# Optimization experiments

Hardware: AMD Instinct MI355X
Metric: run time of the kernel (lower is better)

## Reference

```python
import jax, jax.numpy as jnp
import numpy as np

EPS = 1e-6

def _rms(x, w):
    # RMSNorm over last dim with learned scale w
    var = jnp.mean(x * x, axis=-1, keepdims=True)
    return x * jax.lax.rsqrt(var + EPS) * w

def _split_heads(x, h):
    b, l, hd = x.shape
    return x.reshape(b, l, h, hd // h).transpose(0, 2, 1, 3)  # b h l d

def setup_inputs() -> dict:
    key = jax.random.key(0)
    ks = jax.random.split(key, 12)
    D = 2048          # hidden_size == ip_hidden_states_dim
    H = 16            # n_heads
    Dh = 128          # head_dim
    T = 1280          # timesteps_emb_dim
    B, L, Lip = 2, 2048, 512
    s = 0.02
    return {
        "ip_hidden_states": jax.random.normal(ks[0], (B, Lip, D), jnp.float32),
        "img_query": jax.random.normal(ks[1], (B, L, D), jnp.float32),
        "img_key": jax.random.normal(ks[2], (B, L, D), jnp.float32),
        "img_value": jax.random.normal(ks[3], (B, L, D), jnp.float32),
        "t_emb": jax.random.normal(ks[4], (B, T), jnp.float32),
        "W_ada": jax.random.normal(ks[5], (2 * D, T), jnp.float32) * s,
        "b_ada": jax.random.normal(ks[6], (2 * D,), jnp.float32) * s,
        "W_k_ip": jax.random.normal(ks[7], (D, D), jnp.float32) * s,
        "W_v_ip": jax.random.normal(ks[8], (D, D), jnp.float32) * s,
        "w_q": jnp.ones((Dh,), jnp.float32),
        "w_k": jnp.ones((Dh,), jnp.float32),
        "w_ipk": jnp.ones((Dh,), jnp.float32),
        "n_heads": H,
    }

def reference(ip_hidden_states, img_query, img_key, img_value, t_emb,
              W_ada, b_ada, W_k_ip, W_v_ip, w_q, w_k, w_ipk, n_heads):
    D = img_query.shape[-1]
    # AdaLayerNorm (mode='normal'): silu -> linear -> shift/scale, LN(no affine)
    emb = jax.nn.silu(t_emb) @ W_ada.T + b_ada          # [B, 2D]
    shift, scale = emb[:, :D], emb[:, D:]
    x = ip_hidden_states
    mu = jnp.mean(x, axis=-1, keepdims=True)
    var = jnp.mean((x - mu) ** 2, axis=-1, keepdims=True)
    xn = (x - mu) * jax.lax.rsqrt(var + 1e-6)
    ip_n = xn * (1.0 + scale[:, None, :]) + shift[:, None, :]
    # K/V projections for IP tokens
    ip_key = ip_n @ W_k_ip.T
    ip_value = ip_n @ W_v_ip.T
    # split heads
    q = _split_heads(img_query, n_heads)   # b h L d
    k = _split_heads(img_key, n_heads)
    v = _split_heads(img_value, n_heads)
    kip = _split_heads(ip_key, n_heads)    # b h Lip d
    vip = _split_heads(ip_value, n_heads)
    # RMSNorms
    q = _rms(q, w_q)
    k = _rms(k, w_k)
    kip = _rms(kip, w_ipk)
    # concat image + IP along sequence
    kcat = jnp.concatenate([k, kip], axis=2)
    vcat = jnp.concatenate([v, vip], axis=2)
    # SDPA
    d = q.shape[-1]
    scores = jnp.einsum('bhld,bhmd->bhlm', q, kcat) / jnp.sqrt(jnp.asarray(d, q.dtype))
    attn = jax.nn.softmax(scores, axis=-1)
    out = jnp.einsum('bhlm,bhmd->bhld', attn, vcat)
    b, h, l, dh = out.shape
    return out.transpose(0, 2, 1, 3).reshape(b, l, h * dh)
```

## Files before the change

kernel.cpp:

```cpp
#include <hip/hip_runtime.h>
#include <hip/hip_bf16.h>

typedef __attribute__((ext_vector_type(8))) __bf16 bf16x8;
typedef __attribute__((ext_vector_type(2))) __bf16 bf16x2;
typedef __attribute__((ext_vector_type(4))) float floatx4;
typedef __attribute__((ext_vector_type(2))) unsigned int uint2v;

#define DEV static __device__ __forceinline__

typedef __attribute__((address_space(1))) const unsigned int gu32;
typedef __attribute__((address_space(3))) unsigned int lu32;

DEV void dma16(const void* g, void* l) {
  __builtin_amdgcn_global_load_lds((gu32*)g, (lu32*)l, 16, 0, 0);
}

DEV unsigned short f2bf(float f) {
  unsigned int u = __float_as_uint(f);
  u += 0x7fffu + ((u >> 16) & 1u);
  return (unsigned short)(u >> 16);
}

DEV unsigned int pk_bf16(float a, float b) {
#if __has_builtin(__builtin_amdgcn_cvt_pk_bf16_f32)
  bf16x2 r = __builtin_amdgcn_cvt_pk_bf16_f32(a, b);
  union { bf16x2 v; unsigned int u; } c; c.v = r;
  return c.u;
#else
  return (unsigned int)f2bf(a) | ((unsigned int)f2bf(b) << 16);
#endif
}

DEV float wred_sum(float v) {
#pragma unroll
  for (int o = 32; o > 0; o >>= 1) v += __shfl_xor(v, o, 64);
  return v;
}

DEV floatx4 mfma32(bf16x8 a, bf16x8 b, floatx4 c) {
  return __builtin_amdgcn_mfma_f32_16x16x32_bf16(a, b, c, 0, 0, 0);
}

#if __has_builtin(__builtin_amdgcn_permlane32_swap) && __has_builtin(__builtin_amdgcn_permlane16_swap)
#define HAS_PLSWAP 1
DEV void p32sw(unsigned int& a, unsigned int& b) {
  uint2v r = __builtin_amdgcn_permlane32_swap(a, b, false, false);
  a = r[0]; b = r[1];
}
DEV void p16sw(unsigned int& a, unsigned int& b) {
  uint2v r = __builtin_amdgcn_permlane16_swap(a, b, false, false);
  a = r[0]; b = r[1];
}
#endif

__global__ void ada_kernel(const float* __restrict__ t_emb, const float* __restrict__ W_ada,
                           const float* __restrict__ b_ada, float* __restrict__ emb) {
  int w = threadIdx.x >> 6, lane = threadIdx.x & 63;
  int gid = blockIdx.x * 4 + w;
  int b = gid >> 12, n = gid & 4095;
  const float* te = t_emb + (size_t)b * 1280;
  const float* wr = W_ada + (size_t)n * 1280;
  float acc = 0.f;
#pragma unroll
  for (int i = 0; i < 20; ++i) {
    int t = lane + i * 64;
    float x = te[t];
    float s = x / (1.f + __expf(-x));
    acc += s * wr[t];
  }
  acc = wred_sum(acc);
  if (lane == 0) emb[gid] = acc + b_ada[n];
}

__global__ void ln_mod_kernel(const float* __restrict__ ip, const float* __restrict__ emb,
                              unsigned short* __restrict__ ipn) {
  int row = blockIdx.x;
  int b = row >> 9;
  const float* x = ip + (size_t)row * 2048;
  float xv[8];
  float s1 = 0.f, s2 = 0.f;
#pragma unroll
  for (int i = 0; i < 8; ++i) {
    float v = x[threadIdx.x + i * 256];
    xv[i] = v; s1 += v; s2 += v * v;
  }
  s1 = wred_sum(s1); s2 = wred_sum(s2);
  __shared__ float r1[4], r2[4];
  int w = threadIdx.x >> 6, lane = threadIdx.x & 63;
  if (lane == 0) { r1[w] = s1; r2[w] = s2; }
  __syncthreads();
  s1 = r1[0] + r1[1] + r1[2] + r1[3];
  s2 = r2[0] + r2[1] + r2[2] + r2[3];
  float mu = s1 * (1.f / 2048.f);
  float var = s2 * (1.f / 2048.f) - mu * mu;
  float rs = rsqrtf(var + 1e-6f);
  const float* sh = emb + (size_t)b * 4096;
  unsigned short* y = ipn + (size_t)row * 2048;
#pragma unroll
  for (int i = 0; i < 8; ++i) {
    int d = threadIdx.x + i * 256;
    float v = (xv[i] - mu) * rs;
    v = v * (1.f + sh[2048 + d]) + sh[d];
    y[d] = f2bf(v);
  }
}

struct us4 { unsigned short a, b, c, d; };
__global__ void cvtw_kernel(const float* __restrict__ wk, const float* __restrict__ wv,
                            unsigned short* __restrict__ wk16, unsigned short* __restrict__ wv16) {
  size_t i = ((size_t)blockIdx.x * 256 + threadIdx.x) * 4;
  float4 a = *(const float4*)(wk + i);
  float4 b = *(const float4*)(wv + i);
  us4 oa = { f2bf(a.x), f2bf(a.y), f2bf(a.z), f2bf(a.w) };
  us4 ob = { f2bf(b.x), f2bf(b.y), f2bf(b.z), f2bf(b.w) };
  *(us4*)(wk16 + i) = oa;
  *(us4*)(wv16 + i) = ob;
}

__global__ __launch_bounds__(256) void proj_gemm(const unsigned short* __restrict__ A,
    const unsigned short* __restrict__ Wk, const unsigned short* __restrict__ Wv,
    float* __restrict__ Ck, float* __restrict__ Cv) {
  const unsigned short* Bm = blockIdx.z ? Wv : Wk;
  float* C = blockIdx.z ? Cv : Ck;
  int n0 = blockIdx.x * 64, m0 = blockIdx.y * 128;
  __shared__ __align__(16) unsigned short As[128 * 72];
  __shared__ __align__(16) unsigned short Bs[64 * 72];
  int tid = threadIdx.x, w = tid >> 6, lane = tid & 63, quad = lane >> 4, l16 = lane & 15;
  floatx4 acc[2][4];
#pragma unroll
  for (int i = 0; i < 2; ++i)
#pragma unroll
    for (int j = 0; j < 4; ++j) { floatx4 z = {0.f, 0.f, 0.f, 0.f}; acc[i][j] = z; }
  for (int kk = 0; kk < 2048; kk += 64) {
#pragma unroll
    for (int it = 0; it < 4; ++it) {
      int idx = tid + it * 256;
      int row = idx >> 3, chk = idx & 7;
      *(uint4*)&As[row * 72 + chk * 8] = *(const uint4*)&A[(size_t)(m0 + row) * 2048 + kk + chk * 8];
    }
#pragma unroll
    for (int it = 0; it < 2; ++it) {
      int idx = tid + it * 256;
      int row = idx >> 3, chk = idx & 7;
      *(uint4*)&Bs[row * 72 + chk * 8] = *(const uint4*)&Bm[(size_t)(n0 + row) * 2048 + kk + chk * 8];
    }
    __syncthreads();
#pragma unroll
    for (int c = 0; c < 2; ++c) {
      bf16x8 a0 = *(const bf16x8*)&As[(w * 32 + l16) * 72 + quad * 8 + c * 32];
      bf16x8 a1 = *(const bf16x8*)&As[(w * 32 + 16 + l16) * 72 + quad * 8 + c * 32];
#pragma unroll
      for (int nt = 0; nt < 4; ++nt) {
        bf16x8 bb = *(const bf16x8*)&Bs[(nt * 16 + l16) * 72 + quad * 8 + c * 32];
        acc[0][nt] = mfma32(a0, bb, acc[0][nt]);
        acc[1][nt] = mfma32(a1, bb, acc[1][nt]);
      }
    }
    __syncthreads();
  }
#pragma unroll
  for (int rt = 0; rt < 2; ++rt)
#pragma unroll
    for (int nt = 0; nt < 4; ++nt)
#pragma unroll
      for (int r = 0; r < 4; ++r)
        C[(size_t)(m0 + w * 32 + rt * 16 + quad * 4 + r) * 2048 + n0 + nt * 16 + l16] = acc[rt][nt][r];
}

__global__ __launch_bounds__(256) void kv_build(const float* __restrict__ img_key, const float* __restrict__ img_value,
                         const float* __restrict__ ipk, const float* __restrict__ ipv,
                         const float* __restrict__ w_k, const float* __restrict__ w_ipk,
                         unsigned short* __restrict__ Kc, unsigned short* __restrict__ VtT) {
  int bh = blockIdx.x;
  int mt = blockIdx.y;
  int b = bh >> 4, hh = bh & 15;
  int m0 = mt * 64;
  __shared__ __align__(16) unsigned short Vs[64 * 132];
  int tid = threadIdx.x;
  int mrow = tid >> 2, dq = tid & 3;
  int m = m0 + mrow;
  size_t base;
  const float* wsrc;
  const float *ksrc, *vsrc;
  if (m < 2048) {
    base = (size_t)(b * 2048 + m) * 2048 + hh * 128;
    ksrc = img_key + base; vsrc = img_value + base; wsrc = w_k;
  } else {
    base = (size_t)(b * 512 + (m - 2048)) * 2048 + hh * 128;
    ksrc = ipk + base; vsrc = ipv + base; wsrc = w_ipk;
  }
  float kvv[32]; float ss = 0.f;
  const float4* k4 = (const float4*)ksrc;
#pragma unroll
  for (int i = 0; i < 8; ++i) {
    float4 x = k4[dq * 8 + i];
    kvv[i * 4 + 0] = x.x; kvv[i * 4 + 1] = x.y; kvv[i * 4 + 2] = x.z; kvv[i * 4 + 3] = x.w;
    ss += x.x * x.x + x.y * x.y + x.z * x.z + x.w * x.w;
  }
  ss += __shfl_xor(ss, 1, 64);
  ss += __shfl_xor(ss, 2, 64);
  float rs = rsqrtf(ss * (1.f / 128.f) + 1e-6f);
  unsigned short kb[32];
#pragma unroll
  for (int j = 0; j < 32; ++j) kb[j] = f2bf(kvv[j] * rs * wsrc[dq * 32 + j]);
  uint4* kdst = (uint4*)&Kc[((size_t)bh * 2560 + m) * 128];
#pragma unroll
  for (int i = 0; i < 4; ++i) kdst[(dq * 4 + i) ^ (m & 7)] = ((const uint4*)kb)[i];
  const float4* v4 = (const float4*)vsrc;
#pragma unroll
  for (int i = 0; i < 8; ++i) {
    float4 x = v4[dq * 8 + i];
    us4 p = { f2bf(x.x), f2bf(x.y), f2bf(x.z), f2bf(x.w) };
    *(us4*)&Vs[mrow * 132 + dq * 32 + i * 4] = p;
  }
  __syncthreads();
  int d = tid >> 1, half = tid & 1;
  unsigned short ob[32];
#pragma unroll
  for (int j = 0; j < 32; ++j) ob[j] = Vs[(half * 32 + j) * 132 + d];
  uint4* vdst = (uint4*)&VtT[((size_t)(bh * 40 + mt)) * 8192 + d * 64];
#pragma unroll
  for (int i = 0; i < 4; ++i) vdst[(half * 4 + i) ^ (d & 7)] = ((const uint4*)ob)[i];
}

__global__ __launch_bounds__(256, 2) void attn_kernel(const float* __restrict__ Qf,
    const float* __restrict__ w_q,
    const unsigned short* __restrict__ Kc, const unsigned short* __restrict__ VtT,
    float* __restrict__ out) {
  const float SCL = 0.12751744f;
  const float FM = 17.0f;
  int n = blockIdx.x;
  int xcd = n & 7, jj = n >> 3;
  int bh = xcd * 4 + (jj >> 5);
  int qt = jj & 31;
  int b = bh >> 4, hh = bh & 15;
  int tid = threadIdx.x, w = tid >> 6, lane = tid & 63, quad = lane >> 4, l16 = lane & 15;
  int qh = w >> 1, mh = w & 1;
  int xr = l16 & 7;

  __shared__ __align__(16) unsigned char smem[65536];
  float* epi = (float*)smem;
  __shared__ float rsl[4][32];

  int q0 = qt * 64;

  bf16x8 aq[2][4];
#pragma unroll
  for (int qtl = 0; qtl < 2; ++qtl) {
    int qrow = q0 + qh * 32 + qtl * 16 + l16;
    const float* src = Qf + ((size_t)(b * 2048 + qrow)) * 2048 + hh * 128;
    float xs[32]; float ss = 0.f;
#pragma unroll
    for (int c = 0; c < 4; ++c) {
      float4 a = *(const float4*)&src[quad * 8 + c * 32];
      float4 b2 = *(const float4*)&src[quad * 8 + c * 32 + 4];
      xs[c * 8 + 0] = a.x;  xs[c * 8 + 1] = a.y;  xs[c * 8 + 2] = a.z;  xs[c * 8 + 3] = a.w;
      xs[c * 8 + 4] = b2.x; xs[c * 8 + 5] = b2.y; xs[c * 8 + 6] = b2.z; xs[c * 8 + 7] = b2.w;
      ss += a.x * a.x + a.y * a.y + a.z * a.z + a.w * a.w
          + b2.x * b2.x + b2.y * b2.y + b2.z * b2.z + b2.w * b2.w;
    }
    ss += __shfl_xor(ss, 16, 64);
    ss += __shfl_xor(ss, 32, 64);
    float rs = rsqrtf(ss * (1.f / 128.f) + 1e-6f);
#pragma unroll
    for (int c = 0; c < 4; ++c) {
      float4 wa = *(const float4*)&w_q[quad * 8 + c * 32];
      float4 wb = *(const float4*)&w_q[quad * 8 + c * 32 + 4];
      union { unsigned int u[4]; bf16x8 v; } pk;
      pk.u[0] = pk_bf16(xs[c * 8 + 0] * rs * wa.x, xs[c * 8 + 1] * rs * wa.y);
      pk.u[1] = pk_bf16(xs[c * 8 + 2] * rs * wa.z, xs[c * 8 + 3] * rs * wa.w);
      pk.u[2] = pk_bf16(xs[c * 8 + 4] * rs * wb.x, xs[c * 8 + 5] * rs * wb.y);
      pk.u[3] = pk_bf16(xs[c * 8 + 6] * rs * wb.z, xs[c * 8 + 7] * rs * wb.w);
      aq[qtl][c] = pk.v;
    }
  }

  const unsigned short* Kb = Kc + (size_t)bh * 2560 * 128;
  const unsigned short* Vb = VtT + (size_t)bh * 40 * 8192;

  floatx4 acc[2][8];
#pragma unroll
  for (int i = 0; i < 2; ++i)
#pragma unroll
    for (int j = 0; j < 8; ++j) { floatx4 z = {0.f, 0.f, 0.f, 0.f}; acc[i][j] = z; }
  float rsum[2] = {0.f, 0.f};

  int seg = w * 4;
  auto stage = [&](int buf, int t) {
    const unsigned short* Ksrc = Kb + (size_t)t * 8192;
    const unsigned short* Vsrc = Vb + (size_t)t * 8192;
    unsigned short* Kt = (unsigned short*)(smem + buf * 32768);
    unsigned short* Vd = (unsigned short*)(smem + buf * 32768 + 16384);
#pragma unroll
    for (int j = 0; j < 4; ++j) {
      int off = (seg + j) * 512 + lane * 8;
      dma16(Ksrc + off, Kt + (seg + j) * 512);
      dma16(Vsrc + off, Vd + (seg + j) * 512);
    }
  };

  stage(0, 0);
  __syncthreads();

  for (int t = 0; t < 40; ++t) {
    int cur = t & 1;
    if (t < 39) stage(cur ^ 1, t + 1);
    const unsigned short* Kt = (const unsigned short*)(smem + cur * 32768);
    const unsigned short* Vs = (const unsigned short*)(smem + cur * 32768 + 16384);

    floatx4 sacc[2][2];
#pragma unroll
    for (int i = 0; i < 2; ++i)
#pragma unroll
      for (int j = 0; j < 2; ++j) { floatx4 z = {0.f, 0.f, 0.f, 0.f}; sacc[i][j] = z; }
#pragma unroll
    for (int nt2 = 0; nt2 < 2; ++nt2) {
      int krow = (mh * 32 + nt2 * 16 + l16) * 128;
#pragma unroll
      for (int c = 0; c < 4; ++c) {
        bf16x8 bk = *(const bf16x8*)&Kt[krow + ((quad + c * 4) ^ xr) * 8];
        sacc[nt2][0] = mfma32(bk, aq[0][c], sacc[nt2][0]);
        sacc[nt2][1] = mfma32(bk, aq[1][c], sacc[nt2][1]);
      }
    }

    union { unsigned int u[4]; bf16x8 v; } pf[2];
#pragma unroll
    for (int qtl = 0; qtl < 2; ++qtl) {
      float pv0[4], pv1[4];
#pragma unroll
      for (int r = 0; r < 4; ++r) {
        pv0[r] = __builtin_amdgcn_exp2f(fmaf(sacc[0][qtl][r], SCL, -FM));
        pv1[r] = __builtin_amdgcn_exp2f(fmaf(sacc[1][qtl][r], SCL, -FM));
      }
      rsum[qtl] += (pv0[0] + pv0[1]) + (pv0[2] + pv0[3])
                 + (pv1[0] + pv1[1]) + (pv1[2] + pv1[3]);
      unsigned int R0 = pk_bf16(pv0[0], pv0[1]);
      unsigned int R1 = pk_bf16(pv0[2], pv0[3]);
      unsigned int R2 = pk_bf16(pv1[0], pv1[1]);
      unsigned int R3 = pk_bf16(pv1[2], pv1[3]);
#ifdef HAS_PLSWAP
      p32sw(R0, R2);
      p32sw(R1, R3);
      p16sw(R0, R2);
      p16sw(R1, R3);
      pf[qtl].u[0] = R0; pf[qtl].u[1] = R1; pf[qtl].u[2] = R2; pf[qtl].u[3] = R3;
#else
      int base = ((quad & 1) * 2) * 16 + l16;
      int base2 = base + 16;
      unsigned int a0 = __shfl((int)R0, base, 64),  b0 = __shfl((int)R2, base, 64);
      unsigned int a1 = __shfl((int)R1, base, 64),  b1 = __shfl((int)R3, base, 64);
      unsigned int a2 = __shfl((int)R0, base2, 64), b2 = __shfl((int)R2, base2, 64);
      unsigned int a3 = __shfl((int)R1, base2, 64), b3 = __shfl((int)R3, base2, 64);
      bool hi = (quad >> 1) != 0;
      pf[qtl].u[0] = hi ? b0 : a0;
      pf[qtl].u[1] = hi ? b1 : a1;
      pf[qtl].u[2] = hi ? b2 : a2;
      pf[qtl].u[3] = hi ? b3 : a3;
#endif
    }

#pragma unroll
    for (int dt = 0; dt < 8; ++dt) {
      bf16x8 va = *(const bf16x8*)&Vs[(dt * 16 + l16) * 64 + (((mh * 4 + quad) ^ xr)) * 8];
      acc[0][dt] = mfma32(va, pf[0].v, acc[0][dt]);
      acc[1][dt] = mfma32(va, pf[1].v, acc[1][dt]);
    }
    __syncthreads();
  }

  rsum[0] += __shfl_xor(rsum[0], 16, 64); rsum[0] += __shfl_xor(rsum[0], 32, 64);
  rsum[1] += __shfl_xor(rsum[1], 16, 64); rsum[1] += __shfl_xor(rsum[1], 32, 64);
  if (quad == 0) { rsl[w][l16] = rsum[0]; rsl[w][16 + l16] = rsum[1]; }
  if (mh == 1) {
#pragma unroll
    for (int qtl = 0; qtl < 2; ++qtl)
#pragma unroll
      for (int dt = 0; dt < 8; ++dt)
        *(floatx4*)&epi[(qh * 32 + qtl * 16 + l16) * 132 + dt * 16 + quad * 4] = acc[qtl][dt];
  }
  __syncthreads();
  if (mh == 0) {
#pragma unroll
    for (int qtl = 0; qtl < 2; ++qtl) {
      float inv = 1.f / (rsum[qtl] + rsl[w + 1][qtl * 16 + l16]);
      int qrow = q0 + qh * 32 + qtl * 16 + l16;
      float* orow = out + ((size_t)(b * 2048 + qrow)) * 2048 + hh * 128;
#pragma unroll
      for (int dt = 0; dt < 8; ++dt) {
        floatx4 part = *(const floatx4*)&epi[(qh * 32 + qtl * 16 + l16) * 132 + dt * 16 + quad * 4];
        floatx4 r = (acc[qtl][dt] + part) * inv;
        *(floatx4*)&orow[dt * 16 + quad * 4] = r;
      }
    }
  }
}

extern "C" void kernel_launch(void* const* d_in, const int* in_sizes, int n_in,
                              void* d_out, int out_size, void* d_ws, size_t ws_size,
                              hipStream_t stream) {
  const float* ip    = (const float*)d_in[0];
  const float* q     = (const float*)d_in[1];
  const float* k     = (const float*)d_in[2];
  const float* v     = (const float*)d_in[3];
  const float* temb  = (const float*)d_in[4];
  const float* wada  = (const float*)d_in[5];
  const float* bada  = (const float*)d_in[6];
  const float* wkip  = (const float*)d_in[7];
  const float* wvip  = (const float*)d_in[8];
  const float* w_q   = (const float*)d_in[9];
  const float* w_k   = (const float*)d_in[10];
  const float* w_ipk = (const float*)d_in[11];
  float* out = (float*)d_out;
  char* ws = (char*)d_ws;

  float* emb           = (float*)(ws + 0);
  unsigned short* ipn  = (unsigned short*)(ws + 32768);
  unsigned short* wk16 = (unsigned short*)(ws + 4227072);
  unsigned short* wv16 = (unsigned short*)(ws + 12615680);
  unsigned short* Kcat = (unsigned short*)(ws + 16777216);
  unsigned short* VtT  = (unsigned short*)(ws + 37748736);
  float* ipk           = (float*)(ws + 58720256);
  float* ipv           = (float*)(ws + 67108864);

  ada_kernel<<<dim3(2048), dim3(256), 0, stream>>>(temb, wada, bada, emb);
  ln_mod_kernel<<<dim3(1024), dim3(256), 0, stream>>>(ip, emb, ipn);
  cvtw_kernel<<<dim3(4096), dim3(256), 0, stream>>>(wkip, wvip, wk16, wv16);
  proj_gemm<<<dim3(32, 8, 2), dim3(256), 0, stream>>>(ipn, wk16, wv16, ipk, ipv);
  kv_build<<<dim3(32, 40), dim3(256), 0, stream>>>(k, v, ipk, ipv, w_k, w_ipk, Kcat, VtT);
  attn_kernel<<<dim3(1024), dim3(256), 0, stream>>>(q, w_q, Kcat, VtT, out);
}
```

Baseline: 406.4 us.

## Give each attention wave full key tile, doubling query rows per block

The attention block now covers 128 query rows instead of 64. Each of the four waves handles 32 query rows across the full 64-key tile, rather than splitting keys between two waves. This doubles the reuse of every staged K/V tile and halves the total K/V traffic from global memory into LDS. It also removes the cross-wave reduction through shared memory in the epilogue. In exchange the grid drops to 512 blocks and each wave holds more score accumulators, which raises register pressure and may reduce occupancy or tail-balance.

```diff
diff --git a/kernel.cpp b/kernel.cpp
--- a/kernel.cpp
+++ b/kernel.cpp
@@ -231,23 +231,20 @@
   const float FM = 17.0f;
   int n = blockIdx.x;
   int xcd = n & 7, jj = n >> 3;
-  int bh = xcd * 4 + (jj >> 5);
-  int qt = jj & 31;
+  int bh = xcd * 4 + (jj >> 4);
+  int qt2 = jj & 15;
   int b = bh >> 4, hh = bh & 15;
   int tid = threadIdx.x, w = tid >> 6, lane = tid & 63, quad = lane >> 4, l16 = lane & 15;
-  int qh = w >> 1, mh = w & 1;
   int xr = l16 & 7;
 
   __shared__ __align__(16) unsigned char smem[65536];
-  float* epi = (float*)smem;
-  __shared__ float rsl[4][32];
-
-  int q0 = qt * 64;
+
+  int q0 = qt2 * 128;
 
   bf16x8 aq[2][4];
 #pragma unroll
   for (int qtl = 0; qtl < 2; ++qtl) {
-    int qrow = q0 + qh * 32 + qtl * 16 + l16;
+    int qrow = q0 + w * 32 + qtl * 16 + l16;
     const float* src = Qf + ((size_t)(b * 2048 + qrow)) * 2048 + hh * 128;
     float xs[32]; float ss = 0.f;
 #pragma unroll
@@ -308,90 +305,86 @@
     const unsigned short* Kt = (const unsigned short*)(smem + cur * 32768);
     const unsigned short* Vs = (const unsigned short*)(smem + cur * 32768 + 16384);
 
-    floatx4 sacc[2][2];
-#pragma unroll
-    for (int i = 0; i < 2; ++i)
-#pragma unroll
-      for (int j = 0; j < 2; ++j) { floatx4 z = {0.f, 0.f, 0.f, 0.f}; sacc[i][j] = z; }
-#pragma unroll
-    for (int nt2 = 0; nt2 < 2; ++nt2) {
-      int krow = (mh * 32 + nt2 * 16 + l16) * 128;
+    floatx4 sacc[4][2];
+#pragma unroll
+    for (int ms = 0; ms < 4; ++ms)
+#pragma unroll
+      for (int j = 0; j < 2; ++j) { floatx4 z = {0.f, 0.f, 0.f, 0.f}; sacc[ms][j] = z; }
+#pragma unroll
+    for (int ms = 0; ms < 4; ++ms) {
+      int krow = (ms * 16 + l16) * 128;
 #pragma unroll
       for (int c = 0; c < 4; ++c) {
         bf16x8 bk = *(const bf16x8*)&Kt[krow + ((quad + c * 4) ^ xr) * 8];
-        sacc[nt2][0] = mfma32(bk, aq[0][c], sacc[nt2][0]);
-        sacc[nt2][1] = mfma32(bk, aq[1][c], sacc[nt2][1]);
+        sacc[ms][0] = mfma32(bk, aq[0][c], sacc[ms][0]);
+        sacc[ms][1] = mfma32(bk, aq[1][c], sacc[ms][1]);
       }
     }
 
-    union { unsigned int u[4]; bf16x8 v; } pf[2];
-#pragma unroll
-    for (int qtl = 0; qtl < 2; ++qtl) {
-      float pv0[4], pv1[4];
-#pragma unroll
-      for (int r = 0; r < 4; ++r) {
-        pv0[r] = __builtin_amdgcn_exp2f(fmaf(sacc[0][qtl][r], SCL, -FM));
-        pv1[r] = __builtin_amdgcn_exp2f(fmaf(sacc[1][qtl][r], SCL, -FM));
+    union { unsigned int u[4]; bf16x8 v; } pf[2][2];
+#pragma unroll
+    for (int mc = 0; mc < 2; ++mc) {
+#pragma unroll
+      for (int qtl = 0; qtl < 2; ++qtl) {
+        float pA[4], pB[4];
+#pragma unroll
+        for (int r = 0; r < 4; ++r) {
+          pA[r] = __builtin_amdgcn_exp2f(fmaf(sacc[mc * 2][qtl][r], SCL, -FM));
+          pB[r] = __builtin_amdgcn_exp2f(fmaf(sacc[mc * 2 + 1][qtl][r], SCL, -FM));
+        }
+        rsum[qtl] += (pA[0] + pA[1]) + (pA[2] + pA[3])
+                   + (pB[0] + pB[1]) + (pB[2] + pB[3]);
+        unsigned int R0 = pk_bf16(pA[0], pA[1]);
+        unsigned int R1 = pk_bf16(pA[2], pA[3]);
+        unsigned int R2 = pk_bf16(pB[0], pB[1]);
+        unsigned int R3 = pk_bf16(pB[2], pB[3]);
+#ifdef HAS_PLSWAP
+        p32sw(R0, R2);
+        p32sw(R1, R3);
+        p16sw(R0, R2);
+        p16sw(R1, R3);
+        pf[mc][qtl].u[0] = R0; pf[mc][qtl].u[1] = R1;
+        pf[mc][qtl].u[2] = R2; pf[mc][qtl].u[3] = R3;
+#else
+        int base = ((quad & 1) * 2) * 16 + l16;
+        int base2 = base + 16;
+        unsigned int a0 = __shfl((int)R0, base, 64),  b0 = __shfl((int)R2, base, 64);
+        unsigned int a1 = __shfl((int)R1, base, 64),  b1 = __shfl((int)R3, base, 64);
+        unsigned int a2 = __shfl((int)R0, base2, 64), b2 = __shfl((int)R2, base2, 64);
+        unsigned int a3 = __shfl((int)R1, base2, 64), b3 = __shfl((int)R3, base2, 64);
+        bool hi = (quad >> 1) != 0;
+        pf[mc][qtl].u[0] = hi ? b0 : a0;
+        pf[mc][qtl].u[1] = hi ? b1 : a1;
+        pf[mc][qtl].u[2] = hi ? b2 : a2;
+        pf[mc][qtl].u[3] = hi ? b3 : a3;
+#endif
       }
-      rsum[qtl] += (pv0[0] + pv0[1]) + (pv0[2] + pv0[3])
-                 + (pv1[0] + pv1[1]) + (pv1[2] + pv1[3]);
-      unsigned int R0 = pk_bf16(pv0[0], pv0[1]);
-      unsigned int R1 = pk_bf16(pv0[2], pv0[3]);
-      unsigned int R2 = pk_bf16(pv1[0], pv1[1]);
-      unsigned int R3 = pk_bf16(pv1[2], pv1[3]);
-#ifdef HAS_PLSWAP
-      p32sw(R0, R2);
-      p32sw(R1, R3);
-      p16sw(R0, R2);
-      p16sw(R1, R3);
-      pf[qtl].u[0] = R0; pf[qtl].u[1] = R1; pf[qtl].u[2] = R2; pf[qtl].u[3] = R3;
-#else
-      int base = ((quad & 1) * 2) * 16 + l16;
-      int base2 = base + 16;
-      unsigned int a0 = __shfl((int)R0, base, 64),  b0 = __shfl((int)R2, base, 64);
-      unsigned int a1 = __shfl((int)R1, base, 64),  b1 = __shfl((int)R3, base, 64);
-      unsigned int a2 = __shfl((int)R0, base2, 64), b2 = __shfl((int)R2, base2, 64);
-      unsigned int a3 = __shfl((int)R1, base2, 64), b3 = __shfl((int)R3, base2, 64);
-      bool hi = (quad >> 1) != 0;
-      pf[qtl].u[0] = hi ? b0 : a0;
-      pf[qtl].u[1] = hi ? b1 : a1;
-      pf[qtl].u[2] = hi ? b2 : a2;
-      pf[qtl].u[3] = hi ? b3 : a3;
-#endif
     }
 
 #pragma unroll
     for (int dt = 0; dt < 8; ++dt) {
-      bf16x8 va = *(const bf16x8*)&Vs[(dt * 16 + l16) * 64 + (((mh * 4 + quad) ^ xr)) * 8];
-      acc[0][dt] = mfma32(va, pf[0].v, acc[0][dt]);
-      acc[1][dt] = mfma32(va, pf[1].v, acc[1][dt]);
+      int vrow = (dt * 16 + l16) * 64;
+#pragma unroll
+      for (int mc = 0; mc < 2; ++mc) {
+        bf16x8 va = *(const bf16x8*)&Vs[vrow + ((mc * 4 + quad) ^ xr) * 8];
+        acc[0][dt] = mfma32(va, pf[mc][0].v, acc[0][dt]);
+        acc[1][dt] = mfma32(va, pf[mc][1].v, acc[1][dt]);
+      }
     }
     __syncthreads();
   }
 
   rsum[0] += __shfl_xor(rsum[0], 16, 64); rsum[0] += __shfl_xor(rsum[0], 32, 64);
   rsum[1] += __shfl_xor(rsum[1], 16, 64); rsum[1] += __shfl_xor(rsum[1], 32, 64);
-  if (quad == 0) { rsl[w][l16] = rsum[0]; rsl[w][16 + l16] = rsum[1]; }
-  if (mh == 1) {
-#pragma unroll
-    for (int qtl = 0; qtl < 2; ++qtl)
-#pragma unroll
-      for (int dt = 0; dt < 8; ++dt)
-        *(floatx4*)&epi[(qh * 32 + qtl * 16 + l16) * 132 + dt * 16 + quad * 4] = acc[qtl][dt];
-  }
-  __syncthreads();
-  if (mh == 0) {
-#pragma unroll
-    for (int qtl = 0; qtl < 2; ++qtl) {
-      float inv = 1.f / (rsum[qtl] + rsl[w + 1][qtl * 16 + l16]);
-      int qrow = q0 + qh * 32 + qtl * 16 + l16;
-      float* orow = out + ((size_t)(b * 2048 + qrow)) * 2048 + hh * 128;
-#pragma unroll
-      for (int dt = 0; dt < 8; ++dt) {
-        floatx4 part = *(const floatx4*)&epi[(qh * 32 + qtl * 16 + l16) * 132 + dt * 16 + quad * 4];
-        floatx4 r = (acc[qtl][dt] + part) * inv;
-        *(floatx4*)&orow[dt * 16 + quad * 4] = r;
-      }
+#pragma unroll
+  for (int qtl = 0; qtl < 2; ++qtl) {
+    float inv = 1.f / rsum[qtl];
+    int qrow = q0 + w * 32 + qtl * 16 + l16;
+    float* orow = out + ((size_t)(b * 2048 + qrow)) * 2048 + hh * 128;
+#pragma unroll
+    for (int dt = 0; dt < 8; ++dt) {
+      floatx4 r = acc[qtl][dt] * inv;
+      *(floatx4*)&orow[dt * 16 + quad * 4] = r;
     }
   }
 }
@@ -428,5 +421,5 @@
   cvtw_kernel<<<dim3(4096), dim3(256), 0, stream>>>(wkip, wvip, wk16, wv16);
   proj_gemm<<<dim3(32, 8, 2), dim3(256), 0, stream>>>(ipn, wk16, wv16, ipk, ipv);
   kv_build<<<dim3(32, 40), dim3(256), 0, stream>>>(k, v, ipk, ipv, w_k, w_ipk, Kcat, VtT);
-  attn_kernel<<<dim3(1024), dim3(256), 0, stream>>>(q, w_q, Kcat, VtT, out);
-}
+  attn_kernel<<<dim3(512), dim3(256), 0, stream>>>(q, w_q, Kcat, VtT, out);
+}
```

Measured after the change: 381.4 us. 6.2% less time.
